# Optimization experiments

Hardware: AMD Instinct MI355X
Metric: run time of the kernel (lower is better)

Reference implementation:

```python
import jax, jax.numpy as jnp
import numpy as np
from jax import lax

MAX_DF = 0.05
MAX_DPHI = 0.5
MAX_DA = 0.5
MIN_LENGTH = 2
B, W, K, C = 16, 128, 32, 9
NEG = -1e30  # sentinel for 'no chain'


def _wrap(x):
    return (x + jnp.pi) % (2 * jnp.pi) - jnp.pi


def _per_batch(tok):  # tok: (W, K, C)
    snr = tok[..., 0]
    ps = tok[..., 7]
    pe = tok[..., 8]
    pos = snr > 0
    karr = jnp.arange(K)
    warr = jnp.arange(W)

    # ---- pairwise edge compatibility E[w, kp, kn], w in 0..W-2 ----
    fe = tok[:-1, :, None, 4]
    fs = tok[1:, None, :, 3]
    fm = (fe + fs) * 0.5
    ok_f = (fm <= 0) | (jnp.abs(fe - fs) / jnp.where(fm > 0, fm, 1.0) <= MAX_DF)
    dphi = _wrap(ps[1:, None, :] - pe[:-1, :, None])
    ok_p = jnp.abs(dphi) <= MAX_DPHI
    ae = tok[:-1, :, None, 6]
    an = tok[1:, None, :, 5]
    am = jnp.maximum(ae, an)
    ok_a = (am <= 0) | (jnp.abs(ae - an) / jnp.where(am > 0, am, 1.0) <= MAX_DA)
    E = pos[:-1, :, None] & pos[1:, None, :] & ok_f & ok_p & ok_a  # (W-1,K,K)

    # ---- DP: best-SNR chain per (w,k); only chains reachable from w=0 extend ----
    def dp(carry, inp):
        best, ext = carry
        Ew, sn = inp
        cand = jnp.where(Ew & ext[:, None], best[:, None], NEG)  # (K,K)
        bf = cand.max(0)
        kp = cand.argmax(0)  # first max == first kp on ties (matches dict update)
        reached = bf > NEG * 0.5
        te = bf + sn
        pn = sn > 0
        tot = jnp.where(reached, te, jnp.where(pn, sn, NEG))
        prv = jnp.where(reached, kp, -1)
        return (jnp.where(reached, te, NEG), reached), (tot, prv)

    init = (jnp.where(pos[0], snr[0], NEG), pos[0])
    _, (tr, pr) = lax.scan(dp, init, (E, snr[1:]))
    totals = jnp.concatenate([init[0][None], tr], 0)  # (W,K)
    prev = jnp.concatenate([jnp.full((1, K), -1), pr], 0)  # (W,K)

    # ---- path matrix P[w,k,w'] = token index occupying window w' (or -1) ----
    base = jnp.where(pos[0][:, None] & (warr == 0)[None, :], karr[:, None], -1)
    def pstep(Pw, inp):
        w1, pv, pw = inp
        rows = jnp.where(pv[:, None] >= 0, Pw[jnp.clip(pv, 0)], -1)
        col = (warr == w1)[None, :]
        rows = jnp.where(col, jnp.where(pw[:, None], karr[:, None], -1), rows)
        return rows, rows
    _, Pr = lax.scan(pstep, base, (jnp.arange(1, W), prev[1:], pos[1:]))
    P = jnp.concatenate([base[None], Pr], 0).reshape(W * K, W)
    N = W * K

    # ---- greedy non-overlapping assignment by total SNR (NMS-like) ----
    tot_f = jnp.where(pos.reshape(N), totals.reshape(N), -jnp.inf)
    order = jnp.argsort(-tot_f)  # stable, descending
    def gstep(used, idx):
        row = P[idx]
        m = (row[:, None] == karr[None, :]) & (row[:, None] >= 0)  # (W,K) slots
        ok = (tot_f[idx] > -jnp.inf) & (~jnp.any(m & used))
        return used | (m & ok), ok
    _, flags = lax.scan(gstep, jnp.zeros((W, K), bool), order)
    selected = jnp.zeros(N, bool).at[order].set(flags)

    # ---- anchors per chain, vectorized over all N chains ----
    occ = P >= 0
    L = occ.sum(1)  # chain length
    w_end = jnp.arange(N) // K
    ws = w_end - L + 1  # start window
    tv = tok[warr[None, :], jnp.clip(P, 0)]  # (N,W,C) gathered per-chain tokens
    bpos = jnp.arange(W + 1)
    start = bpos[None, :] == ws[:, None]
    end = bpos[None, :] == (w_end + 1)[:, None]
    ws_c = jnp.clip(ws, 0, W - 1)[:, None]

    def mid(xs, xe):  # boundary anchor values over absolute positions b=0..W
        xsv = jnp.take_along_axis(xs, ws_c, 1)
        xev = jnp.take_along_axis(xe, w_end[:, None], 1)
        inter = (jnp.pad(xe, ((0, 0), (1, 0))) + jnp.pad(xs, ((0, 0), (0, 1)))) * 0.5
        return jnp.where(start, xsv, jnp.where(end, xev, inter))

    a_t = mid(tv[..., 1], tv[..., 2])
    a_f = mid(tv[..., 3], tv[..., 4])
    a_A = mid(tv[..., 5], tv[..., 6])

    # phase: ps[ws] + cumulative within-window advances + boundary corrections
    psv = tv[..., 7]
    pev = tv[..., 8]
    pe_m1 = jnp.pad(pev, ((0, 0), (1, 0)))[:, :W]
    d_gen = _wrap(psv - pe_m1) + pev - psv
    d_first = pev - psv
    j = warr[None, :]
    in_rng = (j >= ws[:, None]) & (j <= w_end[:, None])
    d = jnp.where(in_rng, jnp.where(j == ws[:, None], d_first, d_gen), 0.0)
    ps0 = jnp.take_along_axis(psv, ws_c, 1)
    a_phi = ps0 + jnp.pad(jnp.cumsum(d, 1), ((0, 0), (1, 0)))

    anch = jnp.stack([a_A, a_t, a_phi, a_f], -1)  # (N, W+1, 4) abs-aligned
    # shift each chain's anchors to start at index 0 (relative alignment)
    pad = jnp.pad(anch, ((0, 0), (0, W), (0, 0)))
    rel = jax.vmap(lambda a, s: lax.dynamic_slice(a, (s, 0), (W + 1, 4)))(pad, jnp.clip(ws, 0, W))
    vmask = jnp.arange(W + 1)[None, :] <= L[:, None]  # anchors 0..L valid
    sel = selected & (L >= MIN_LENGTH)
    return rel * (sel[:, None, None] & vmask[:, :, None]).astype(rel.dtype)


def setup_inputs() -> dict:
    key = jax.random.key(0)
    tokens = jax.random.uniform(key, (B, W, K, C), dtype=jnp.float32)
    return {"tokens": tokens}


def reference(tokens):
    return jax.vmap(_per_batch)(tokens)
```

## Files before the change

### kernel.cpp

```cpp
#include <hip/hip_runtime.h>

#define WN 128
#define KN 32
#define CN 9
#define NBND 129
#define NEGF (-1e30f)
#define CW 8
#define NFILL 2048
#define PIf 3.14159265358979323846f


__global__ __launch_bounds__(256, 1) void fused_kernel(const float* __restrict__ tok,
                                                       float4* __restrict__ anchors,
                                                       int* __restrict__ meta,
                                                       float4* __restrict__ outz,
                                                       long total4, int B) {
    const int bid = blockIdx.x;
    const int t = threadIdx.x;

    if (bid >= B) {
        long i = (long)(bid - B) * 256 + t;
        const long stride = (long)NFILL * 256;
        float4 z = make_float4(0.f, 0.f, 0.f, 0.f);
        for (; i < total4; i += stride) outz[i] = z;
        return;
    }

    const int b = bid;
    const float* T = tok + (size_t)b * WN * KN * CN;

    __shared__ float sm_tok[(CW + 1) * KN * CN];
    __shared__ unsigned sm_cmask[CW * KN];
    __shared__ unsigned sm_cun[CW];
    __shared__ signed char sm_prev[WN * KN];
    __shared__ unsigned long long s_key[KN];
    __shared__ unsigned char s_path[KN][WN];
    __shared__ float s_d[KN][NBND];
    __shared__ int s_we[KN];
    __shared__ int s_e[KN];
    __shared__ int s_alive;
    __shared__ int s_wstop;

    if (t < KN) { s_key[t] = 0ull; s_we[t] = -1; }
    if (t == 0) { s_alive = 1; s_wstop = WN; }

    float best = NEGF;
    int root = 0;

    for (int c0 = 1; c0 < WN; c0 += CW) {
        const int cend = (c0 + CW < WN) ? (c0 + CW) : WN;
        const int cn = cend - c0;

        {
            const float4* src = (const float4*)(T + (size_t)(c0 - 1) * KN * CN);
            float4* dst = (float4*)sm_tok;
            const int nf4 = (cn + 1) * (KN * CN / 4);
            for (int j = t; j < nf4; j += 256) dst[j] = src[j];
        }
        if (t < CW) sm_cun[t] = 0u;
        __syncthreads();

        {
            const int kp = t & 31;
            const int half = (t >> 5) & 1;
            const int wave = t >> 6;
            for (int m2 = wave * 2; m2 < cn * KN; m2 += 8) {
                const int m = m2 + half;
                const int ci = m >> 5;
                const int kn = m & 31;
                const float* Tp = &sm_tok[ci * (KN * CN) + kp * CN];
                const float* Tc = &sm_tok[(ci + 1) * (KN * CN) + kn * CN];
                float fe = Tp[4], fs = Tc[3];
                float fm = (fe + fs) * 0.5f;
                bool ok_f = (fm <= 0.0f) || (fabsf(fe - fs) / (fm > 0.0f ? fm : 1.0f) <= 0.05f);
                float aw = (Tc[7] - Tp[8]) + PIf;
                float dphi = aw - PIf;
                bool ok_p = fabsf(dphi) <= 0.5f;
                float ae = Tp[6], an = Tc[5];
                float am = fmaxf(ae, an);
                bool ok_a = (am <= 0.0f) || (fabsf(ae - an) / (am > 0.0f ? am : 1.0f) <= 0.5f);
                bool ok = (Tp[0] > 0.0f) && (Tc[0] > 0.0f) && ok_f && ok_p && ok_a;
                unsigned long long bal = __ballot(ok);
                unsigned lo = (unsigned)bal, hi = (unsigned)(bal >> 32);
                int lw = t & 63;
                if (lw == 0) {
                    sm_cmask[m2] = lo;
                    if (lo) atomicOr(&sm_cun[m2 >> 5], lo);
                } else if (lw == 32) {
                    sm_cmask[m2 + 1] = hi;
                    if (hi) atomicOr(&sm_cun[(m2 + 1) >> 5], hi);
                }
            }
        }
        __syncthreads();

        if (t < 64) {
            __builtin_amdgcn_s_setprio(1);
            const int kn = t & 31;
            if (c0 == 1) {
                float s0 = sm_tok[kn * CN + 0];
                best = (s0 > 0.0f) ? s0 : NEGF;
                root = kn;
            }
            bool died = false;
            for (int w = c0; w < cend; ++w) {
                if (__ballot(best > NEGF) == 0ull) {
                    died = true;
                    if (t == 0) { s_alive = 0; s_wstop = w; }
                    break;
                }
                const int ci = w - c0;
                unsigned mask = sm_cmask[ci * KN + kn];
                float sn = sm_tok[(ci + 1) * (KN * CN) + kn * CN + 0];
                unsigned un = (unsigned)__builtin_amdgcn_readfirstlane((int)sm_cun[ci]);
                float v = NEGF;
                int idx = 0, nr = 0;
                while (un) {
                    int i = __builtin_amdgcn_readfirstlane(__builtin_ctz(un));
                    un &= un - 1u;
                    float bv = __int_as_float(
                        __builtin_amdgcn_readlane(__float_as_int(best), i));
                    int rv = __builtin_amdgcn_readlane(root, i);
                    bool c = ((mask >> i) & 1u) && (bv > v);
                    v = c ? bv : v;
                    idx = c ? i : idx;
                    nr = c ? rv : nr;
                }
                bool reached = v > -5e29f;
                float te = v + sn;
                if (t < 32) sm_prev[w * KN + kn] = reached ? (signed char)idx : (signed char)-1;
                if (reached) {
                    root = nr;
                    best = te;
                    if (t < 32) {
                        unsigned ubk = __float_as_uint(te);
                        ubk ^= (ubk >> 31) ? 0xFFFFFFFFu : 0x80000000u;
                        unsigned e = (unsigned)(w * KN + kn);
                        unsigned long long key = ((unsigned long long)ubk << 32)
                                               | (unsigned long long)(0xFFFFFFFFu - e);
                        atomicMax(&s_key[root], key);
                    }
                } else {
                    best = NEGF;
                }
            }
            if (!died) {
                if (__ballot(best > NEGF) == 0ull) {
                    if (t == 0) { s_alive = 0; s_wstop = cend; }
                }
            }
            __builtin_amdgcn_s_setprio(0);
        }
        __syncthreads();
        if (!s_alive) break;
    }

    {
        const int wstop = s_wstop;
        for (int i2 = wstop * KN + t; i2 < WN * KN; i2 += 256)
            sm_prev[i2] = (signed char)-1;
    }
    __syncthreads();

    if (t < KN) {
        unsigned long long key = s_key[t];
        int we = -1, e = -1;
        if (key != 0ull) {
            e = (int)(0xFFFFFFFFu - (unsigned)(key & 0xFFFFFFFFull));
            we = e >> 5;
            int k = e & 31;
            for (int ww = we; ww > 0; --ww) {
                s_path[t][ww] = (unsigned char)k;
                k = sm_prev[ww * KN + k];
            }
            s_path[t][0] = (unsigned char)k;
        }
        s_we[t] = we;
        s_e[t] = e;
        meta[b * KN + t] = we;
        meta[(size_t)B * KN + b * KN + t] = e;
    }
    __syncthreads();

    for (int u = t; u < KN * NBND; u += 256) {
        int r = u / NBND, bp = u - r * NBND;
        int we = s_we[r];
        if (we < 0) continue;
        if (bp <= we) {
            float dv;
            int pj = s_path[r][bp];
            if (bp == 0) {
                const float* Tq = T + pj * CN;
                dv = Tq[8] - Tq[7];
            } else {
                int pm = s_path[r][bp - 1];
                float pe_prev = T[((bp - 1) * KN + pm) * CN + 8];
                float psj = T[(bp * KN + pj) * CN + 7];
                float pej = T[(bp * KN + pj) * CN + 8];
                float aw = (psj - pe_prev) + PIf;
                dv = (aw - PIf) + pej - psj;
            }
            s_d[r][bp] = dv;
        }
        int L = we + 1;
        if (bp <= L) {
            float aA, at, af;
            if (bp == 0) {
                const float* Tq = T + (int)s_path[r][0] * CN;
                at = Tq[1]; af = Tq[3]; aA = Tq[5];
            } else if (bp == L) {
                const float* Tq = T + (we * KN + (int)s_path[r][we]) * CN;
                at = Tq[2]; af = Tq[4]; aA = Tq[6];
            } else {
                const float* Ta = T + ((bp - 1) * KN + (int)s_path[r][bp - 1]) * CN;
                const float* Tb = T + (bp * KN + (int)s_path[r][bp]) * CN;
                at = (Ta[2] + Tb[1]) * 0.5f;
                af = (Ta[4] + Tb[3]) * 0.5f;
                aA = (Ta[6] + Tb[5]) * 0.5f;
            }
            float* arow = (float*)(anchors + ((size_t)b * KN + r) * NBND + bp);
            arow[0] = aA; arow[1] = at; arow[3] = af;
        }
    }
    __syncthreads();

    if (t < KN && s_we[t] >= 0) {
        int we = s_we[t];
        int p0 = s_path[t][0];
        float cum = T[p0 * CN + 7];
        float* arow = (float*)(anchors + ((size_t)b * KN + t) * NBND);
        arow[2] = cum;
        for (int j = 0; j <= we; ++j) {
            cum += s_d[t][j];
            arow[(j + 1) * 4 + 2] = cum;
        }
    }
}

__global__ __launch_bounds__(256) void scatter_kernel(const float4* __restrict__ anchors,
                                                      const int* __restrict__ meta,
                                                      float4* __restrict__ out, int B) {
    const int b = blockIdx.x;
    const int t = threadIdx.x;
    for (int u = t; u < KN * NBND; u += 256) {
        int r = u / NBND, bp = u - r * NBND;
        int we = meta[b * KN + r];
        if (we < 0 || bp > we + 1) continue;
        int e = meta[(size_t)B * KN + b * KN + r];
        out[((size_t)b * (WN * KN) + e) * NBND + bp] =
            anchors[((size_t)b * KN + r) * NBND + bp];
    }
}

extern "C" void kernel_launch(void* const* d_in, const int* in_sizes, int n_in,
                              void* d_out, int out_size, void* d_ws, size_t ws_size,
                              hipStream_t stream) {
    const float* tok = (const float*)d_in[0];
    int B = in_sizes[0] / (WN * KN * CN);

    size_t off = 0;
    float4* anchors = (float4*)d_ws;
    off += (size_t)B * KN * NBND * sizeof(float4);
    off = (off + 255) & ~(size_t)255;
    int* meta = (int*)((char*)d_ws + off);

    long total4 = (long)out_size / 4;

    hipLaunchKernelGGL(fused_kernel, dim3(B + NFILL), dim3(256), 0, stream,
                       tok, anchors, meta, (float4*)d_out, total4, B);
    hipLaunchKernelGGL(scatter_kernel, dim3(B), dim3(256), 0, stream,
                       anchors, meta, (float4*)d_out, B);
}
```

Baseline: 65.02 us.

## Write anchors directly to output and zero it with hipMemsetAsync

Drops the workspace anchor buffer and the separate scatter kernel; the DP kernel now writes each chain's anchors straight to its final output row, indexed by its end token. The zero-fill blocks that used to run inside the fused kernel are replaced by a hipMemsetAsync before the launch, and the block size goes from 256 to 512 threads. This removes one kernel launch and the round trip through the workspace. The catch is that the large output zeroing now runs before the DP work instead of overlapping with it.

```diff
diff --git a/kernel.cpp b/kernel.cpp
--- a/kernel.cpp
+++ b/kernel.cpp
@@ -6,27 +6,14 @@
 #define NBND 129
 #define NEGF (-1e30f)
 #define CW 8
-#define NFILL 2048
+#define TPB 512
 #define PIf 3.14159265358979323846f
 
 
-__global__ __launch_bounds__(256, 1) void fused_kernel(const float* __restrict__ tok,
-                                                       float4* __restrict__ anchors,
-                                                       int* __restrict__ meta,
-                                                       float4* __restrict__ outz,
-                                                       long total4, int B) {
-    const int bid = blockIdx.x;
+__global__ __launch_bounds__(TPB) void dp_kernel(const float* __restrict__ tok,
+                                                 float* __restrict__ out) {
+    const int b = blockIdx.x;
     const int t = threadIdx.x;
-
-    if (bid >= B) {
-        long i = (long)(bid - B) * 256 + t;
-        const long stride = (long)NFILL * 256;
-        float4 z = make_float4(0.f, 0.f, 0.f, 0.f);
-        for (; i < total4; i += stride) outz[i] = z;
-        return;
-    }
-
-    const int b = bid;
     const float* T = tok + (size_t)b * WN * KN * CN;
 
     __shared__ float sm_tok[(CW + 1) * KN * CN];
@@ -55,7 +42,7 @@
             const float4* src = (const float4*)(T + (size_t)(c0 - 1) * KN * CN);
             float4* dst = (float4*)sm_tok;
             const int nf4 = (cn + 1) * (KN * CN / 4);
-            for (int j = t; j < nf4; j += 256) dst[j] = src[j];
+            for (int j = t; j < nf4; j += TPB) dst[j] = src[j];
         }
         if (t < CW) sm_cun[t] = 0u;
         __syncthreads();
@@ -64,7 +51,7 @@
             const int kp = t & 31;
             const int half = (t >> 5) & 1;
             const int wave = t >> 6;
-            for (int m2 = wave * 2; m2 < cn * KN; m2 += 8) {
+            for (int m2 = wave * 2; m2 < cn * KN; m2 += 2 * (TPB / 64)) {
                 const int m = m2 + half;
                 const int ci = m >> 5;
                 const int kn = m & 31;
@@ -157,7 +144,7 @@
 
     {
         const int wstop = s_wstop;
-        for (int i2 = wstop * KN + t; i2 < WN * KN; i2 += 256)
+        for (int i2 = wstop * KN + t; i2 < WN * KN; i2 += TPB)
             sm_prev[i2] = (signed char)-1;
     }
     __syncthreads();
@@ -177,12 +164,11 @@
         }
         s_we[t] = we;
         s_e[t] = e;
-        meta[b * KN + t] = we;
-        meta[(size_t)B * KN + b * KN + t] = e;
     }
     __syncthreads();
 
-    for (int u = t; u < KN * NBND; u += 256) {
+    float* Ob = out + (size_t)b * (WN * KN) * NBND * 4;
+    for (int u = t; u < KN * NBND; u += TPB) {
         int r = u / NBND, bp = u - r * NBND;
         int we = s_we[r];
         if (we < 0) continue;
@@ -218,7 +204,7 @@
                 af = (Ta[4] + Tb[3]) * 0.5f;
                 aA = (Ta[6] + Tb[5]) * 0.5f;
             }
-            float* arow = (float*)(anchors + ((size_t)b * KN + r) * NBND + bp);
+            float* arow = Ob + ((size_t)s_e[r] * NBND + bp) * 4;
             arow[0] = aA; arow[1] = at; arow[3] = af;
         }
     }
@@ -228,27 +214,12 @@
         int we = s_we[t];
         int p0 = s_path[t][0];
         float cum = T[p0 * CN + 7];
-        float* arow = (float*)(anchors + ((size_t)b * KN + t) * NBND);
+        float* arow = Ob + (size_t)s_e[t] * NBND * 4;
         arow[2] = cum;
         for (int j = 0; j <= we; ++j) {
             cum += s_d[t][j];
             arow[(j + 1) * 4 + 2] = cum;
         }
-    }
-}
-
-__global__ __launch_bounds__(256) void scatter_kernel(const float4* __restrict__ anchors,
-                                                      const int* __restrict__ meta,
-                                                      float4* __restrict__ out, int B) {
-    const int b = blockIdx.x;
-    const int t = threadIdx.x;
-    for (int u = t; u < KN * NBND; u += 256) {
-        int r = u / NBND, bp = u - r * NBND;
-        int we = meta[b * KN + r];
-        if (we < 0 || bp > we + 1) continue;
-        int e = meta[(size_t)B * KN + b * KN + r];
-        out[((size_t)b * (WN * KN) + e) * NBND + bp] =
-            anchors[((size_t)b * KN + r) * NBND + bp];
     }
 }
 
@@ -258,16 +229,6 @@
     const float* tok = (const float*)d_in[0];
     int B = in_sizes[0] / (WN * KN * CN);
 
-    size_t off = 0;
-    float4* anchors = (float4*)d_ws;
-    off += (size_t)B * KN * NBND * sizeof(float4);
-    off = (off + 255) & ~(size_t)255;
-    int* meta = (int*)((char*)d_ws + off);
-
-    long total4 = (long)out_size / 4;
-
-    hipLaunchKernelGGL(fused_kernel, dim3(B + NFILL), dim3(256), 0, stream,
-                       tok, anchors, meta, (float4*)d_out, total4, B);
-    hipLaunchKernelGGL(scatter_kernel, dim3(B), dim3(256), 0, stream,
-                       anchors, meta, (float4*)d_out, B);
+    hipMemsetAsync(d_out, 0, (size_t)out_size * sizeof(float), stream);
+    hipLaunchKernelGGL(dp_kernel, dim3(B), dim3(TPB), 0, stream, tok, (float*)d_out);
 }
```

Measured after the change: 53.39 us. -17.9%, faster.
